# Performance work log

Measured on AMD Instinct MI355X. Metric: run time of the kernel, lower is better.

Reference implementation:

```python
import jax, jax.numpy as jnp
import numpy as np

DMODEL = 1024
DK = 64
DHEAD = 16
DEPTH = DK * DHEAD
N, LQ, L = 4, 4096, 4096
FAC1 = 1.0 / np.sqrt(DK)  # relu kernel scale folded into omega, as in reset()
EPS = 1e-6


def setup_inputs() -> dict:
    key = jax.random.key(0)
    ks = jax.random.split(key, 10)
    x = jax.random.normal(ks[0], (N, LQ, DMODEL), jnp.float32)
    y = jax.random.normal(ks[1], (N, L, DMODEL), jnp.float32)
    s_in = 1.0 / np.sqrt(DMODEL)
    s_depth = 1.0 / np.sqrt(DEPTH)
    # Linear weights stored as (in, out) so application is x @ W + b
    WQ = jax.random.normal(ks[2], (DMODEL, DEPTH), jnp.float32) * s_in
    WK = jax.random.normal(ks[3], (DMODEL, DEPTH), jnp.float32) * s_in
    WV = jax.random.normal(ks[4], (DMODEL, DEPTH), jnp.float32) * s_in
    WO = jax.random.normal(ks[5], (DEPTH, DMODEL), jnp.float32) * s_depth
    bQ = jnp.zeros((DEPTH,), jnp.float32)
    bK = jnp.zeros((DEPTH,), jnp.float32)
    bV = jnp.zeros((DEPTH,), jnp.float32)
    bO = jnp.zeros((DMODEL,), jnp.float32)
    # orthogonal random-feature projection: QR of gaussian, scaled by sqrt(dk), then *fac1 (relu)
    g = np.random.default_rng(0).standard_normal((DK, DK)).astype(np.float32)
    qmat, _ = np.linalg.qr(g)
    omega = jnp.asarray(qmat * np.sqrt(DK) * FAC1, dtype=jnp.float32)
    return dict(x=x, y=y, WQ=WQ, bQ=bQ, WK=WK, bK=bK, WV=WV, bV=bV,
                WO=WO, bO=bO, omega=omega)


def reference(x, y, WQ, bQ, WK, bK, WV, bV, WO, bO, omega):
    n, lq, _ = x.shape
    l = y.shape[1]
    # project and split heads: (n, h, L, dk)
    q = (x @ WQ + bQ).reshape(n, lq, DHEAD, DK).transpose(0, 2, 1, 3)
    k = (y @ WK + bK).reshape(n, l, DHEAD, DK).transpose(0, 2, 1, 3)
    v = (y @ WV + bV).reshape(n, l, DHEAD, DK).transpose(0, 2, 1, 3)
    # relu random-feature map phi(x) = relu(x @ omega) + eps
    q = jax.nn.relu(q @ omega) + EPS
    k = jax.nn.relu(k @ omega) + EPS
    # linear attention: out = phi(q) @ (phi(k)^T @ v) / (phi(q) @ phi(k)^T @ 1)
    kv = jnp.einsum('nhld,nhle->nhde', k, v)          # (n, h, dk, dk)
    ksum = jnp.sum(k, axis=2)                          # (n, h, dk)
    d_inv = jnp.einsum('nhqd,nhd->nhq', q, ksum)[..., None]
    out = jnp.einsum('nhqd,nhde->nhqe', q, kv) / d_inv  # (n, h, Lq, dk)
    out = out.transpose(0, 2, 1, 3).reshape(n, lq, DEPTH)
    return out @ WO + bO
```

## Files before the change

### kernel.cpp

```cpp
#include <hip/hip_runtime.h>

#define EPSF 1e-6f

typedef _Float16 f16x8 __attribute__((ext_vector_type(8)));
typedef _Float16 f16x4 __attribute__((ext_vector_type(4)));
typedef float    f32x4 __attribute__((ext_vector_type(4)));

#define GLL16(gp, lp) __builtin_amdgcn_global_load_lds( \
    (const __attribute__((address_space(1))) void*)(gp), \
    (__attribute__((address_space(3))) void*)(lp), 16, 0, 0)

__global__ __launch_bounds__(256) void cvt2_f16(const float* __restrict__ inA,
                                                _Float16* __restrict__ outA,
                                                const float* __restrict__ inB,
                                                _Float16* __restrict__ outB, int n8each) {
    int idx = blockIdx.x * 256 + threadIdx.x;
    const float* in = inA; _Float16* out = outA;
    if (idx >= n8each) { idx -= n8each; in = inB; out = outB; }
    const float4* p = (const float4*)in + (size_t)idx * 2;
    float4 a = p[0], b = p[1];
    f16x8 o;
    o[0] = (_Float16)a.x; o[1] = (_Float16)a.y; o[2] = (_Float16)a.z; o[3] = (_Float16)a.w;
    o[4] = (_Float16)b.x; o[5] = (_Float16)b.y; o[6] = (_Float16)b.z; o[7] = (_Float16)b.w;
    *(f16x8*)(out + (size_t)idx * 8) = o;
}

__global__ __launch_bounds__(256) void prep_all(const float* __restrict__ omega,
                                                const float* __restrict__ bQ,
                                                const float* __restrict__ bK,
                                                const float* __restrict__ bV,
                                                _Float16* __restrict__ obdT,
                                                float* __restrict__ bQf,
                                                float* __restrict__ bkv,
                                                float* __restrict__ ksum) {
    int idx = blockIdx.x * 256 + threadIdx.x;
    int c = idx >> 10, k = idx & 1023;
    float v = ((c >> 6) == (k >> 6)) ? omega[(k & 63) * 64 + (c & 63)] : 0.f;
    obdT[idx] = (_Float16)v;
    if (idx < 4096) ksum[idx] = 0.f;
    if (idx < 1024) {
        int h = idx >> 6, e = idx & 63;
        float sq = 0.f, sk = 0.f;
        for (int d = 0; d < 64; d++) {
            float o = omega[d * 64 + e];
            sq += bQ[h * 64 + d] * o;
            sk += bK[h * 64 + d] * o;
        }
        bQf[idx] = sq;
        bkv[h * 128 + e] = sk;
        bkv[h * 128 + 64 + e] = bV[idx];
    }
}

__global__ __launch_bounds__(256) void transpose_cvt(const float* __restrict__ in,
                                                     _Float16* __restrict__ out, int vmode) {
    __shared__ float tile[64][65];
    const int t = threadIdx.x;
    const int k0 = blockIdx.x * 64, n0 = blockIdx.y * 64;
#pragma unroll
    for (int j = 0; j < 16; j++) {
        int idx = j * 256 + t; int r = idx >> 6, c = idx & 63;
        tile[r][c] = in[(size_t)(k0 + r) * 1024 + n0 + c];
    }
    __syncthreads();
#pragma unroll
    for (int j = 0; j < 16; j++) {
        int idx = j * 256 + t; int rn = idx >> 6, ck = idx & 63;
        int rowo = n0 + rn;
        if (vmode) rowo = ((rowo >> 6) << 7) + 64 + (rowo & 63);
        out[(size_t)rowo * 1024 + k0 + ck] = (_Float16)tile[ck][rn];
    }
}

__global__ __launch_bounds__(256) void gemm_fold(const _Float16* __restrict__ A,
                                                 const _Float16* __restrict__ Bt,
                                                 _Float16* __restrict__ out0,
                                                 _Float16* __restrict__ out1) {
    const int K = 1024;
    __shared__ __align__(16) _Float16 Asm[128 * 32];
    __shared__ __align__(16) _Float16 Bsm[128 * 32];
    const int t = threadIdx.x, lane = t & 63, w = t >> 6;
    const int bm = blockIdx.y * 128, bn = blockIdx.x * 128;
    const int wm = (w >> 1) * 64, wn = (w & 1) * 64;
    const int r15 = lane & 15, slog = lane >> 4;

    int aoff[4], boff[4];
#pragma unroll
    for (int m = 0; m < 4; m++) {
        int ra = wm + m * 16 + r15;
        aoff[m] = ra * 32 + (slog ^ ((ra >> 1) & 3)) * 8;
        int rb = wn + m * 16 + r15;
        boff[m] = rb * 32 + (slog ^ ((rb >> 1) & 3)) * 8;
    }
    f32x4 acc[4][4];
#pragma unroll
    for (int m = 0; m < 4; m++)
#pragma unroll
        for (int n = 0; n < 4; n++) acc[m][n] = (f32x4){0.f, 0.f, 0.f, 0.f};

    for (int kt = 0; kt < K; kt += 32) {
        __syncthreads();
#pragma unroll
        for (int i = 0; i < 2; i++) {
            int seg = i * 256 + w * 64 + lane;
            int r = seg >> 2, sp = seg & 3;
            int sg = sp ^ ((r >> 1) & 3);
            GLL16(A  + (size_t)(bm + r) * K + kt + sg * 8, Asm + (size_t)(i * 256 + w * 64) * 8);
            GLL16(Bt + (size_t)(bn + r) * K + kt + sg * 8, Bsm + (size_t)(i * 256 + w * 64) * 8);
        }
        __syncthreads();
        f16x8 av[4], bv[4];
#pragma unroll
        for (int m = 0; m < 4; m++) av[m] = *(const f16x8*)(Asm + aoff[m]);
#pragma unroll
        for (int n = 0; n < 4; n++) bv[n] = *(const f16x8*)(Bsm + boff[n]);
#pragma unroll
        for (int m = 0; m < 4; m++)
#pragma unroll
            for (int n = 0; n < 4; n++)
                acc[m][n] = __builtin_amdgcn_mfma_f32_16x16x32_f16(av[m], bv[n], acc[m][n], 0, 0, 0);
    }

#pragma unroll
    for (int m = 0; m < 4; m++) {
        int row0 = bm + wm + m * 16 + slog * 4;
        int l = row0 & 1023;
#pragma unroll
        for (int n = 0; n < 4; n++) {
            int colg = bn + wn + n * 16 + r15;
            f16x4 p;
#pragma unroll
            for (int j = 0; j < 4; j++) p[j] = (_Float16)acc[m][n][j];
            if (row0 < 1024) {
                *(f16x4*)(out0 + (size_t)colg * 1024 + l) = p;
            } else {
                int rr = ((colg >> 6) << 7) + (colg & 63);
                *(f16x4*)(out1 + (size_t)rr * 1024 + l) = p;
            }
        }
    }
}

template<int EPI>
__global__ __launch_bounds__(512, 2) void gemm256(const _Float16* __restrict__ A,
                                                  const _Float16* __restrict__ Bt,
                                                  const float* __restrict__ bias,
                                                  void* __restrict__ out0,
                                                  void* __restrict__ out1,
                                                  float* __restrict__ ksum,
                                                  int M, int N, int K, int nbn) {
    __shared__ __align__(16) char lds[131072];
    const int t = threadIdx.x, lane = t & 63, w = t >> 6;
    const int nwg = gridDim.x;
    const int f = (blockIdx.x & 7) * (nwg >> 3) + (blockIdx.x >> 3);
    const int bm = (f / nbn) * 256, bn = (f % nbn) * 256;
    const int wm = (w & 1) * 128, wn = (w >> 1) * 64;
    const int r15 = lane & 15, hi = lane >> 4;
    const int srow = lane >> 2, sp = lane & 3;
    const _Float16* BtU = (EPI == 2) ? Bt + ((size_t)(bm >> 12) << 20) : Bt;

    int aoff[8], boff[4];
#pragma unroll
    for (int m = 0; m < 8; m++) {
        int r = wm + m * 16 + r15;
        aoff[m] = r * 64 + (((hi + (r >> 1)) & 3) << 4);
    }
#pragma unroll
    for (int n = 0; n < 4; n++) {
        int r = wn + n * 16 + r15;
        boff[n] = r * 64 + (((hi + (r >> 1)) & 3) << 4);
    }

    f32x4 acc[8][4];
#pragma unroll
    for (int m = 0; m < 8; m++)
#pragma unroll
        for (int n = 0; n < 4; n++) acc[m][n] = (f32x4){0.f, 0.f, 0.f, 0.f};

    auto stage = [&](int s) {
        char* base = lds + (s & 3) * 32768;
        int kt = s * 32;
#pragma unroll
        for (int p = 0; p < 2; p++) {
            int row = w * 32 + p * 16 + srow;
            int sg = (sp - ((row >> 1) & 3)) & 3;
            GLL16(A   + (size_t)(bm + row) * K + kt + sg * 8, base + w * 2048 + p * 1024);
            GLL16(BtU + (size_t)(bn + row) * K + kt + sg * 8, base + 16384 + w * 2048 + p * 1024);
        }
    };

    const int NS = K >> 5;
    stage(0); stage(1); stage(2);
    for (int s = 0; s < NS; ++s) {
        if (s + 2 < NS)      asm volatile("s_waitcnt vmcnt(8)" ::: "memory");
        else if (s + 1 < NS) asm volatile("s_waitcnt vmcnt(4)" ::: "memory");
        else                 asm volatile("s_waitcnt vmcnt(0)" ::: "memory");
        asm volatile("s_barrier" ::: "memory");
        if (s + 3 < NS) stage(s + 3);
        const char* La = lds + (s & 3) * 32768;
        const char* Lb = La + 16384;
        f16x8 bv[4];
#pragma unroll
        for (int n = 0; n < 4; n++) bv[n] = *(const f16x8*)(Lb + boff[n]);
        f16x8 av[8];
#pragma unroll
        for (int m = 0; m < 8; m++) av[m] = *(const f16x8*)(La + aoff[m]);
        __builtin_amdgcn_s_setprio(1);
#pragma unroll
        for (int m = 0; m < 8; m++)
#pragma unroll
            for (int n = 0; n < 4; n++)
                acc[m][n] = __builtin_amdgcn_mfma_f32_16x16x32_f16(av[m], bv[n], acc[m][n], 0, 0, 0);
        __builtin_amdgcn_s_setprio(0);
    }

    if (EPI == 5) {
        const int q = w >> 1;
        const bool isK = !(q & 1);
        const int nb = bm >> 12;
        const int g0 = bn >> 7;
        __syncthreads();
        char* LT = lds + q * 32768;
        float cs[4] = {0.f, 0.f, 0.f, 0.f};
#pragma unroll
        for (int m = 0; m < 8; m++)
#pragma unroll
            for (int n = 0; n < 4; n++) {
                int dd = n * 16 + r15;
                float bs = bias[bn + wn + dd];
                f16x4 pk;
#pragma unroll
                for (int j = 0; j < 4; j++) {
                    float xv = acc[m][n][j] + bs;
                    if (isK) { xv = fmaxf(xv, 0.f) + EPSF; cs[n] += xv; }
                    pk[j] = (_Float16)xv;
                }
                int l2 = (wm + m * 16 + hi * 4) * 2;
                *(f16x4*)(LT + dd * 512 + (l2 ^ ((dd & 7) << 4))) = pk;
            }
        if (isK) {
#pragma unroll
            for (int n = 0; n < 4; n++) {
                cs[n] += __shfl_xor(cs[n], 16, 64);
                cs[n] += __shfl_xor(cs[n], 32, 64);
            }
            if (hi == 0) {
#pragma unroll
                for (int n = 0; n < 4; n++)
                    atomicAdd(ksum + (size_t)(nb * 16 + g0 + (q >> 1)) * 64 + n * 16 + r15, cs[n]);
            }
        }
        __syncthreads();
        f32x4 kva[4];
#pragma unroll
        for (int i = 0; i < 4; i++) kva[i] = (f32x4){0.f, 0.f, 0.f, 0.f};
#pragma unroll
        for (int i = 0; i < 4; i++) {
            int tt = w * 4 + i;
            int hl = tt >> 4, dg = (tt >> 2) & 3, eg = tt & 3;
            const char* KT = lds + (hl * 2) * 32768;
            const char* VT = lds + (hl * 2 + 1) * 32768;
            int d = dg * 16 + r15, e = eg * 16 + r15;
#pragma unroll
            for (int ks = 0; ks < 8; ks++) {
                int l2 = (ks * 32 + hi * 8) * 2;
                f16x8 ka = *(const f16x8*)(KT + d * 512 + (l2 ^ ((d & 7) << 4)));
                f16x8 vb = *(const f16x8*)(VT + e * 512 + (l2 ^ ((e & 7) << 4)));
                kva[i] = __builtin_amdgcn_mfma_f32_16x16x32_f16(ka, vb, kva[i], 0, 0, 0);
            }
        }
        const int chunk = (bm >> 8) & 15;
        float* kvp = (float*)out0;
#pragma unroll
        for (int i = 0; i < 4; i++) {
            int tt = w * 4 + i;
            int hl = tt >> 4, dg = (tt >> 2) & 3, eg = tt & 3;
            float* dst = kvp + ((size_t)(nb * 16 + g0 + hl) * 16 + chunk) * 4096;
#pragma unroll
            for (int j = 0; j < 4; j++)
                dst[(dg * 16 + hi * 4 + j) * 64 + eg * 16 + r15] = kva[i][j];
        }
    } else if (EPI == 4) {
        const int headg = (bm >> 12) * 16 + ((bn + wn) >> 6);
        const float* ks = (const float*)out1;
        float ksn[4];
#pragma unroll
        for (int n = 0; n < 4; n++) ksn[n] = ks[(size_t)headg * 64 + n * 16 + r15];
        _Float16* C = (_Float16*)out0;
#pragma unroll
        for (int m = 0; m < 8; m++) {
            int row0 = bm + wm + m * 16 + hi * 4;
            float qv[4][4], dp[4] = {0.f, 0.f, 0.f, 0.f};
#pragma unroll
            for (int n = 0; n < 4; n++) {
                int colg = bn + wn + n * 16 + r15;
                float bs = bias[colg];
#pragma unroll
                for (int j = 0; j < 4; j++) {
                    float xv = fmaxf(acc[m][n][j] + bs, 0.f) + EPSF;
                    qv[n][j] = xv;
                    dp[j] += xv * ksn[n];
                }
            }
#pragma unroll
            for (int j = 0; j < 4; j++) {
                dp[j] += __shfl_xor(dp[j], 1, 64);
                dp[j] += __shfl_xor(dp[j], 2, 64);
                dp[j] += __shfl_xor(dp[j], 4, 64);
                dp[j] += __shfl_xor(dp[j], 8, 64);
                dp[j] = 4096.0f * __builtin_amdgcn_rcpf(dp[j]);
            }
#pragma unroll
            for (int n = 0; n < 4; n++) {
                int colg = bn + wn + n * 16 + r15;
#pragma unroll
                for (int j = 0; j < 4; j++)
                    C[(size_t)(row0 + j) * N + colg] = (_Float16)(qv[n][j] * dp[j]);
            }
        }
    } else {
#pragma unroll
        for (int m = 0; m < 8; m++) {
            int row0 = bm + wm + m * 16 + hi * 4;
#pragma unroll
            for (int n = 0; n < 4; n++) {
                int colg = bn + wn + n * 16 + r15;
                float bs = bias ? bias[colg] : 0.f;
#pragma unroll
                for (int j = 0; j < 4; j++)
                    ((float*)out0)[(size_t)(row0 + j) * N + colg] = acc[m][n][j] + bs;
            }
        }
    }
}

__global__ __launch_bounds__(256) void kvred16(const float* __restrict__ kvpart,
                                               float* __restrict__ kvT) {
    int gh = blockIdx.x, t = threadIdx.x;
    const float* kp = kvpart + (size_t)gh * 16 * 4096;
#pragma unroll
    for (int i = 0; i < 16; i++) {
        int idx = i * 256 + t;
        float s = 0.f;
#pragma unroll
        for (int c = 0; c < 16; c++) s += kp[c * 4096 + idx];
        kvT[(size_t)gh * 4096 + idx] = s;
    }
}

__global__ __launch_bounds__(256) void w2t_kernel(const _Float16* __restrict__ Wot,
                                                  const float* __restrict__ kvT,
                                                  _Float16* __restrict__ W2t) {
    const int t = threadIdx.x;
    const int jb = blockIdx.x;
    const int gh = blockIdx.y;
    const int b = gh >> 4, hl = gh & 15;
    __shared__ float kvL[64][65];
    const float* kp = kvT + (size_t)gh * 4096;
#pragma unroll
    for (int i = 0; i < 16; i++) {
        int idx = i * 256 + t;
        kvL[idx & 63][idx >> 6] = kp[idx];
    }
    __syncthreads();
    const int j = jb * 128 + (t >> 1);
    const int d0 = (t & 1) * 32;
    const _Float16* wr = Wot + (size_t)j * 1024 + hl * 64;
    float wv[64];
#pragma unroll
    for (int i = 0; i < 8; i++) {
        f16x8 v = *(const f16x8*)(wr + i * 8);
#pragma unroll
        for (int k = 0; k < 8; k++) wv[i * 8 + k] = (float)v[k];
    }
    _Float16* outp = W2t + ((size_t)b << 20) + (size_t)j * 1024 + hl * 64 + d0;
#pragma unroll
    for (int d = 0; d < 32; d++) {
        float s = 0.f;
#pragma unroll
        for (int e = 0; e < 64; e++) s += wv[e] * kvL[e][d0 + d];
        outp[d] = (_Float16)(s * (1.0f / 4096.0f));
    }
}

extern "C" void kernel_launch(void* const* d_in, const int* in_sizes, int n_in,
                              void* d_out, int out_size, void* d_ws, size_t ws_size,
                              hipStream_t stream) {
    (void)in_sizes; (void)n_in; (void)out_size; (void)ws_size;
    const float* x     = (const float*)d_in[0];
    const float* y     = (const float*)d_in[1];
    const float* WQ    = (const float*)d_in[2];
    const float* bQ    = (const float*)d_in[3];
    const float* WK    = (const float*)d_in[4];
    const float* bK    = (const float*)d_in[5];
    const float* WV    = (const float*)d_in[6];
    const float* bV    = (const float*)d_in[7];
    const float* WO    = (const float*)d_in[8];
    const float* bO    = (const float*)d_in[9];
    const float* omega = (const float*)d_in[10];

    char* ws = (char*)d_ws;
    size_t off = 0;
    auto alloc = [&](size_t bytes) { void* p = ws + off; off += (bytes + 255) & ~(size_t)255; return p; };
    const size_t BIG = (size_t)16384 * 1024 * 2;
    _Float16* xb    = (_Float16*)alloc(BIG);
    _Float16* yb    = (_Float16*)alloc(BIG);
    _Float16* WQKb  = (_Float16*)alloc((size_t)2048 * 1024 * 2);
    _Float16* obdT  = (_Float16*)alloc(1024 * 1024 * 2);
    _Float16* Wqt   = (_Float16*)alloc(1024 * 1024 * 2);
    _Float16* Wkvt  = (_Float16*)alloc((size_t)2048 * 1024 * 2);
    _Float16* Wot   = (_Float16*)alloc(1024 * 1024 * 2);
    _Float16* W2t   = (_Float16*)alloc((size_t)4 * 1024 * 1024 * 2);
    float*    bQf   = (float*)alloc(1024 * 4);
    float*    bkv   = (float*)alloc(2048 * 4);
    _Float16* U2    = (_Float16*)alloc(BIG);
    float*    kvpart= (float*)alloc((size_t)64 * 16 * 4096 * 4);
    float*    kvT   = (float*)alloc((size_t)64 * 4096 * 4);
    float*    ksum  = (float*)alloc((size_t)64 * 64 * 4);

    cvt2_f16<<<16384, 256, 0, stream>>>(x, xb, y, yb, 16384 * 1024 / 8);
    cvt2_f16<<<1024, 256, 0, stream>>>(WQ, WQKb, WK, WQKb + (size_t)1024 * 1024, 1024 * 1024 / 8);
    prep_all<<<4096, 256, 0, stream>>>(omega, bQ, bK, bV, obdT, bQf, bkv, ksum);
    transpose_cvt<<<dim3(16, 16), 256, 0, stream>>>(WV, Wkvt, 1);
    transpose_cvt<<<dim3(16, 16), 256, 0, stream>>>(WO, Wot, 0);
    gemm_fold<<<dim3(8, 16), 256, 0, stream>>>(WQKb, obdT, Wqt, Wkvt);
    gemm256<5><<<512, 512, 0, stream>>>(yb, Wkvt, bkv, kvpart, nullptr, ksum, 16384, 2048, 1024, 8);
    kvred16<<<64, 256, 0, stream>>>(kvpart, kvT);
    w2t_kernel<<<dim3(8, 64), 256, 0, stream>>>(Wot, kvT, W2t);
    gemm256<4><<<256, 512, 0, stream>>>(xb, Wqt, bQf, U2, ksum, nullptr, 16384, 1024, 1024, 4);
    gemm256<2><<<256, 512, 0, stream>>>(U2, W2t, bO, d_out, nullptr, nullptr, 16384, 1024, 1024, 4);
}
```

Measured before the change: 261.3 us.

## Shrink GEMM tile to 128x256 with double-buffered LDS for higher occupancy

Halves the M tile of the shared GEMM kernel from 256 to 128 rows, cuts LDS from 128KB to 48KB with a 2-stage instead of 4-stage pipeline, and raises launch bounds to allow more resident workgroups. Grid sizes double, and the fused KV epilogue is restructured to process two heads sequentially in reduced LDS, producing 32 partial chunks per head reduced by a new kvred32 kernel. The aim is better latency hiding via occupancy and more workgroups, at the cost of less data reuse per tile, a shallower prefetch pipeline with a full vmcnt(0) wait each step, and twice the partial-KV traffic.

Result: slower. 289.6 us (+10.8%).

```diff
diff --git a/kernel.cpp b/kernel.cpp
--- a/kernel.cpp
+++ b/kernel.cpp
@@ -142,26 +142,25 @@
 }
 
 template<int EPI>
-__global__ __launch_bounds__(512, 2) void gemm256(const _Float16* __restrict__ A,
+__global__ __launch_bounds__(512, 4) void gemm256(const _Float16* __restrict__ A,
                                                   const _Float16* __restrict__ Bt,
                                                   const float* __restrict__ bias,
                                                   void* __restrict__ out0,
                                                   void* __restrict__ out1,
                                                   float* __restrict__ ksum,
                                                   int M, int N, int K, int nbn) {
-    __shared__ __align__(16) char lds[131072];
+    __shared__ __align__(16) char lds[49152];
     const int t = threadIdx.x, lane = t & 63, w = t >> 6;
     const int nwg = gridDim.x;
     const int f = (blockIdx.x & 7) * (nwg >> 3) + (blockIdx.x >> 3);
-    const int bm = (f / nbn) * 256, bn = (f % nbn) * 256;
-    const int wm = (w & 1) * 128, wn = (w >> 1) * 64;
+    const int bm = (f / nbn) * 128, bn = (f % nbn) * 256;
+    const int wm = (w & 1) * 64, wn = (w >> 1) * 64;
     const int r15 = lane & 15, hi = lane >> 4;
-    const int srow = lane >> 2, sp = lane & 3;
     const _Float16* BtU = (EPI == 2) ? Bt + ((size_t)(bm >> 12) << 20) : Bt;
 
-    int aoff[8], boff[4];
-#pragma unroll
-    for (int m = 0; m < 8; m++) {
+    int aoff[4], boff[4];
+#pragma unroll
+    for (int m = 0; m < 4; m++) {
         int r = wm + m * 16 + r15;
         aoff[m] = r * 64 + (((hi + (r >> 1)) & 3) << 4);
     }
@@ -171,43 +170,45 @@
         boff[n] = r * 64 + (((hi + (r >> 1)) & 3) << 4);
     }
 
-    f32x4 acc[8][4];
-#pragma unroll
-    for (int m = 0; m < 8; m++)
+    f32x4 acc[4][4];
+#pragma unroll
+    for (int m = 0; m < 4; m++)
 #pragma unroll
         for (int n = 0; n < 4; n++) acc[m][n] = (f32x4){0.f, 0.f, 0.f, 0.f};
 
     auto stage = [&](int s) {
-        char* base = lds + (s & 3) * 32768;
+        char* base = lds + (s & 1) * 24576;
         int kt = s * 32;
+        {
+            int row = t >> 2;
+            int sg = ((t & 3) - ((row >> 1) & 3)) & 3;
+            GLL16(A + (size_t)(bm + row) * K + kt + sg * 8, base + (size_t)t * 16);
+        }
 #pragma unroll
         for (int p = 0; p < 2; p++) {
-            int row = w * 32 + p * 16 + srow;
-            int sg = (sp - ((row >> 1) & 3)) & 3;
-            GLL16(A   + (size_t)(bm + row) * K + kt + sg * 8, base + w * 2048 + p * 1024);
-            GLL16(BtU + (size_t)(bn + row) * K + kt + sg * 8, base + 16384 + w * 2048 + p * 1024);
+            int seg = p * 512 + t;
+            int row = seg >> 2;
+            int sg = ((seg & 3) - ((row >> 1) & 3)) & 3;
+            GLL16(BtU + (size_t)(bn + row) * K + kt + sg * 8, base + 8192 + (size_t)seg * 16);
         }
     };
 
     const int NS = K >> 5;
-    stage(0); stage(1); stage(2);
+    stage(0);
     for (int s = 0; s < NS; ++s) {
-        if (s + 2 < NS)      asm volatile("s_waitcnt vmcnt(8)" ::: "memory");
-        else if (s + 1 < NS) asm volatile("s_waitcnt vmcnt(4)" ::: "memory");
-        else                 asm volatile("s_waitcnt vmcnt(0)" ::: "memory");
+        asm volatile("s_waitcnt vmcnt(0)" ::: "memory");
         asm volatile("s_barrier" ::: "memory");
-        if (s + 3 < NS) stage(s + 3);
-        const char* La = lds + (s & 3) * 32768;
-        const char* Lb = La + 16384;
-        f16x8 bv[4];
+        if (s + 1 < NS) stage(s + 1);
+        const char* La = lds + (s & 1) * 24576;
+        const char* Lb = La + 8192;
+        f16x8 bv[4], av[4];
 #pragma unroll
         for (int n = 0; n < 4; n++) bv[n] = *(const f16x8*)(Lb + boff[n]);
-        f16x8 av[8];
-#pragma unroll
-        for (int m = 0; m < 8; m++) av[m] = *(const f16x8*)(La + aoff[m]);
+#pragma unroll
+        for (int m = 0; m < 4; m++) av[m] = *(const f16x8*)(La + aoff[m]);
         __builtin_amdgcn_s_setprio(1);
 #pragma unroll
-        for (int m = 0; m < 8; m++)
+        for (int m = 0; m < 4; m++)
 #pragma unroll
             for (int n = 0; n < 4; n++)
                 acc[m][n] = __builtin_amdgcn_mfma_f32_16x16x32_f16(av[m], bv[n], acc[m][n], 0, 0, 0);
@@ -215,70 +216,74 @@
     }
 
     if (EPI == 5) {
-        const int q = w >> 1;
-        const bool isK = !(q & 1);
         const int nb = bm >> 12;
         const int g0 = bn >> 7;
-        __syncthreads();
-        char* LT = lds + q * 32768;
-        float cs[4] = {0.f, 0.f, 0.f, 0.f};
-#pragma unroll
-        for (int m = 0; m < 8; m++)
-#pragma unroll
-            for (int n = 0; n < 4; n++) {
-                int dd = n * 16 + r15;
-                float bs = bias[bn + wn + dd];
-                f16x4 pk;
-#pragma unroll
-                for (int j = 0; j < 4; j++) {
-                    float xv = acc[m][n][j] + bs;
-                    if (isK) { xv = fmaxf(xv, 0.f) + EPSF; cs[n] += xv; }
-                    pk[j] = (_Float16)xv;
+        const int chunk = (bm >> 7) & 31;
+        const int cg = w >> 1;
+        const bool isK = (cg & 1) == 0;
+        asm volatile("s_waitcnt vmcnt(0)" ::: "memory");
+        for (int hp = 0; hp < 2; hp++) {
+            if (hp) { asm volatile("s_barrier" ::: "memory"); }
+            if ((w >> 2) == hp) {
+                char* LT = lds + (cg & 1) * 16384;
+                float cs[4] = {0.f, 0.f, 0.f, 0.f};
+#pragma unroll
+                for (int m = 0; m < 4; m++)
+#pragma unroll
+                    for (int n = 0; n < 4; n++) {
+                        int dd = n * 16 + r15;
+                        float bs = bias[bn + wn + dd];
+                        f16x4 pk;
+#pragma unroll
+                        for (int j = 0; j < 4; j++) {
+                            float xv = acc[m][n][j] + bs;
+                            if (isK) { xv = fmaxf(xv, 0.f) + EPSF; cs[n] += xv; }
+                            pk[j] = (_Float16)xv;
+                        }
+                        int l2 = (wm + m * 16 + hi * 4) * 2;
+                        *(f16x4*)(LT + dd * 256 + (l2 ^ ((dd & 15) << 4))) = pk;
+                    }
+                if (isK) {
+#pragma unroll
+                    for (int n = 0; n < 4; n++) {
+                        cs[n] += __shfl_xor(cs[n], 16, 64);
+                        cs[n] += __shfl_xor(cs[n], 32, 64);
+                    }
+                    if (hi == 0) {
+#pragma unroll
+                        for (int n = 0; n < 4; n++)
+                            atomicAdd(ksum + (size_t)(nb * 16 + g0 + hp) * 64 + n * 16 + r15, cs[n]);
+                    }
                 }
-                int l2 = (wm + m * 16 + hi * 4) * 2;
-                *(f16x4*)(LT + dd * 512 + (l2 ^ ((dd & 7) << 4))) = pk;
-            }
-        if (isK) {
-#pragma unroll
-            for (int n = 0; n < 4; n++) {
-                cs[n] += __shfl_xor(cs[n], 16, 64);
-                cs[n] += __shfl_xor(cs[n], 32, 64);
-            }
-            if (hi == 0) {
-#pragma unroll
-                for (int n = 0; n < 4; n++)
-                    atomicAdd(ksum + (size_t)(nb * 16 + g0 + (q >> 1)) * 64 + n * 16 + r15, cs[n]);
-            }
-        }
-        __syncthreads();
-        f32x4 kva[4];
-#pragma unroll
-        for (int i = 0; i < 4; i++) kva[i] = (f32x4){0.f, 0.f, 0.f, 0.f};
-#pragma unroll
-        for (int i = 0; i < 4; i++) {
-            int tt = w * 4 + i;
-            int hl = tt >> 4, dg = (tt >> 2) & 3, eg = tt & 3;
-            const char* KT = lds + (hl * 2) * 32768;
-            const char* VT = lds + (hl * 2 + 1) * 32768;
-            int d = dg * 16 + r15, e = eg * 16 + r15;
-#pragma unroll
-            for (int ks = 0; ks < 8; ks++) {
-                int l2 = (ks * 32 + hi * 8) * 2;
-                f16x8 ka = *(const f16x8*)(KT + d * 512 + (l2 ^ ((d & 7) << 4)));
-                f16x8 vb = *(const f16x8*)(VT + e * 512 + (l2 ^ ((e & 7) << 4)));
-                kva[i] = __builtin_amdgcn_mfma_f32_16x16x32_f16(ka, vb, kva[i], 0, 0, 0);
-            }
-        }
-        const int chunk = (bm >> 8) & 15;
-        float* kvp = (float*)out0;
-#pragma unroll
-        for (int i = 0; i < 4; i++) {
-            int tt = w * 4 + i;
-            int hl = tt >> 4, dg = (tt >> 2) & 3, eg = tt & 3;
-            float* dst = kvp + ((size_t)(nb * 16 + g0 + hl) * 16 + chunk) * 4096;
-#pragma unroll
-            for (int j = 0; j < 4; j++)
-                dst[(dg * 16 + hi * 4 + j) * 64 + eg * 16 + r15] = kva[i][j];
+            }
+            asm volatile("s_barrier" ::: "memory");
+            const char* KT = lds;
+            const char* VT = lds + 16384;
+            f32x4 kva[2];
+            kva[0] = (f32x4){0.f, 0.f, 0.f, 0.f};
+            kva[1] = (f32x4){0.f, 0.f, 0.f, 0.f};
+#pragma unroll
+            for (int i = 0; i < 2; i++) {
+                int tt = w * 2 + i;
+                int dg = tt >> 2, eg = tt & 3;
+                int d = dg * 16 + r15, e = eg * 16 + r15;
+#pragma unroll
+                for (int ks = 0; ks < 4; ks++) {
+                    int l2 = ks * 64 + hi * 16;
+                    f16x8 ka = *(const f16x8*)(KT + d * 256 + (l2 ^ ((d & 15) << 4)));
+                    f16x8 vb = *(const f16x8*)(VT + e * 256 + (l2 ^ ((e & 15) << 4)));
+                    kva[i] = __builtin_amdgcn_mfma_f32_16x16x32_f16(ka, vb, kva[i], 0, 0, 0);
+                }
+            }
+            float* dst = (float*)out0 + ((size_t)(nb * 16 + g0 + hp) * 32 + chunk) * 4096;
+#pragma unroll
+            for (int i = 0; i < 2; i++) {
+                int tt = w * 2 + i;
+                int dg = tt >> 2, eg = tt & 3;
+#pragma unroll
+                for (int j = 0; j < 4; j++)
+                    dst[(dg * 16 + hi * 4 + j) * 64 + eg * 16 + r15] = kva[i][j];
+            }
         }
     } else if (EPI == 4) {
         const int headg = (bm >> 12) * 16 + ((bn + wn) >> 6);
@@ -288,7 +293,7 @@
         for (int n = 0; n < 4; n++) ksn[n] = ks[(size_t)headg * 64 + n * 16 + r15];
         _Float16* C = (_Float16*)out0;
 #pragma unroll
-        for (int m = 0; m < 8; m++) {
+        for (int m = 0; m < 4; m++) {
             int row0 = bm + wm + m * 16 + hi * 4;
             float qv[4][4], dp[4] = {0.f, 0.f, 0.f, 0.f};
 #pragma unroll
@@ -320,7 +325,7 @@
         }
     } else {
 #pragma unroll
-        for (int m = 0; m < 8; m++) {
+        for (int m = 0; m < 4; m++) {
             int row0 = bm + wm + m * 16 + hi * 4;
 #pragma unroll
             for (int n = 0; n < 4; n++) {
@@ -334,16 +339,16 @@
     }
 }
 
-__global__ __launch_bounds__(256) void kvred16(const float* __restrict__ kvpart,
+__global__ __launch_bounds__(256) void kvred32(const float* __restrict__ kvpart,
                                                float* __restrict__ kvT) {
     int gh = blockIdx.x, t = threadIdx.x;
-    const float* kp = kvpart + (size_t)gh * 16 * 4096;
+    const float* kp = kvpart + (size_t)gh * 32 * 4096;
 #pragma unroll
     for (int i = 0; i < 16; i++) {
         int idx = i * 256 + t;
         float s = 0.f;
 #pragma unroll
-        for (int c = 0; c < 16; c++) s += kp[c * 4096 + idx];
+        for (int c = 0; c < 32; c++) s += kp[c * 4096 + idx];
         kvT[(size_t)gh * 4096 + idx] = s;
     }
 }
@@ -414,7 +419,7 @@
     float*    bQf   = (float*)alloc(1024 * 4);
     float*    bkv   = (float*)alloc(2048 * 4);
     _Float16* U2    = (_Float16*)alloc(BIG);
-    float*    kvpart= (float*)alloc((size_t)64 * 16 * 4096 * 4);
+    float*    kvpart= (float*)alloc((size_t)64 * 32 * 4096 * 4);
     float*    kvT   = (float*)alloc((size_t)64 * 4096 * 4);
     float*    ksum  = (float*)alloc((size_t)64 * 64 * 4);
 
@@ -424,9 +429,9 @@
     transpose_cvt<<<dim3(16, 16), 256, 0, stream>>>(WV, Wkvt, 1);
     transpose_cvt<<<dim3(16, 16), 256, 0, stream>>>(WO, Wot, 0);
     gemm_fold<<<dim3(8, 16), 256, 0, stream>>>(WQKb, obdT, Wqt, Wkvt);
-    gemm256<5><<<512, 512, 0, stream>>>(yb, Wkvt, bkv, kvpart, nullptr, ksum, 16384, 2048, 1024, 8);
-    kvred16<<<64, 256, 0, stream>>>(kvpart, kvT);
+    gemm256<5><<<1024, 512, 0, stream>>>(yb, Wkvt, bkv, kvpart, nullptr, ksum, 16384, 2048, 1024, 8);
+    kvred32<<<64, 256, 0, stream>>>(kvpart, kvT);
     w2t_kernel<<<dim3(8, 64), 256, 0, stream>>>(Wot, kvT, W2t);
-    gemm256<4><<<256, 512, 0, stream>>>(xb, Wqt, bQf, U2, ksum, nullptr, 16384, 1024, 1024, 4);
-    gemm256<2><<<256, 512, 0, stream>>>(U2, W2t, bO, d_out, nullptr, nullptr, 16384, 1024, 1024, 4);
-}
+    gemm256<4><<<512, 512, 0, stream>>>(xb, Wqt, bQf, U2, ksum, nullptr, 16384, 1024, 1024, 4);
+    gemm256<2><<<512, 512, 0, stream>>>(U2, W2t, bO, d_out, nullptr, nullptr, 16384, 1024, 1024, 4);
+}
```

## Restructure GEMM main loop into 8-wave ping-pong phases with split A/B staging

Applied to the files above, without the earlier changes.

Replaces the 4-stage 32-wide K pipeline with 64-wide K tiles that are double-buffered and split into A/B and K-half sub-stages. Each tile is processed in four phases that interleave LDS reads, issue of the next global-to-LDS loads, barriers, and an MFMA cluster over half the M fragments. The goal is to overlap memory issue with MFMA work more finely and to spread LDS traffic across phases. In exchange there are more barriers per K step, and the hand-written vmcnt accounting must match the number of loads in flight.

After: 269.1 us. 1.03x slower.

```diff
diff --git a/kernel.cpp b/kernel.cpp
--- a/kernel.cpp
+++ b/kernel.cpp
@@ -156,7 +156,6 @@
     const int bm = (f / nbn) * 256, bn = (f % nbn) * 256;
     const int wm = (w & 1) * 128, wn = (w >> 1) * 64;
     const int r15 = lane & 15, hi = lane >> 4;
-    const int srow = lane >> 2, sp = lane & 3;
     const _Float16* BtU = (EPI == 2) ? Bt + ((size_t)(bm >> 12) << 20) : Bt;
 
     int aoff[8], boff[4];
@@ -177,41 +176,61 @@
 #pragma unroll
         for (int n = 0; n < 4; n++) acc[m][n] = (f32x4){0.f, 0.f, 0.f, 0.f};
 
-    auto stage = [&](int s) {
-        char* base = lds + (s & 3) * 32768;
-        int kt = s * 32;
+    auto stage = [&](int T, int kh, int isB) {
+        const _Float16* src = isB ? BtU : A;
+        const int brow = isB ? bn : bm;
+        char* base = lds + isB * 65536 + (T & 1) * 32768 + kh * 16384;
+        const int kt = T * 64 + kh * 32;
 #pragma unroll
         for (int p = 0; p < 2; p++) {
-            int row = w * 32 + p * 16 + srow;
-            int sg = (sp - ((row >> 1) & 3)) & 3;
-            GLL16(A   + (size_t)(bm + row) * K + kt + sg * 8, base + w * 2048 + p * 1024);
-            GLL16(BtU + (size_t)(bn + row) * K + kt + sg * 8, base + 16384 + w * 2048 + p * 1024);
+            int seg = p * 512 + t;
+            int row = seg >> 2;
+            int sg = ((seg & 3) - ((row >> 1) & 3)) & 3;
+            GLL16(src + (size_t)(brow + row) * K + kt + sg * 8, base + (size_t)seg * 16);
         }
     };
 
-    const int NS = K >> 5;
-    stage(0); stage(1); stage(2);
-    for (int s = 0; s < NS; ++s) {
-        if (s + 2 < NS)      asm volatile("s_waitcnt vmcnt(8)" ::: "memory");
-        else if (s + 1 < NS) asm volatile("s_waitcnt vmcnt(4)" ::: "memory");
-        else                 asm volatile("s_waitcnt vmcnt(0)" ::: "memory");
-        asm volatile("s_barrier" ::: "memory");
-        if (s + 3 < NS) stage(s + 3);
-        const char* La = lds + (s & 3) * 32768;
-        const char* Lb = La + 16384;
-        f16x8 bv[4];
-#pragma unroll
-        for (int n = 0; n < 4; n++) bv[n] = *(const f16x8*)(Lb + boff[n]);
-        f16x8 av[8];
-#pragma unroll
-        for (int m = 0; m < 8; m++) av[m] = *(const f16x8*)(La + aoff[m]);
-        __builtin_amdgcn_s_setprio(1);
-#pragma unroll
-        for (int m = 0; m < 8; m++)
-#pragma unroll
-            for (int n = 0; n < 4; n++)
-                acc[m][n] = __builtin_amdgcn_mfma_f32_16x16x32_f16(av[m], bv[n], acc[m][n], 0, 0, 0);
-        __builtin_amdgcn_s_setprio(0);
+    const int NT = K >> 6;
+    stage(0, 0, 0); stage(0, 0, 1); stage(0, 1, 0); stage(0, 1, 1);
+    stage(1, 0, 0); stage(1, 0, 1);
+    asm volatile("s_waitcnt vmcnt(4)" ::: "memory");
+    asm volatile("s_barrier" ::: "memory");
+
+    for (int T = 0; T < NT; ++T) {
+        const int b = T & 1;
+        const bool s1 = (T + 1 < NT), s2 = (T + 2 < NT);
+#pragma unroll
+        for (int ph = 0; ph < 4; ph++) {
+            const int kh = ph >> 1, mh = ph & 1;
+            const char* RA = lds + b * 32768 + kh * 16384;
+            const char* RB = RA + 65536;
+            f16x8 av[4], bv[4];
+#pragma unroll
+            for (int i = 0; i < 4; i++) av[i] = *(const f16x8*)(RA + aoff[mh * 4 + i]);
+#pragma unroll
+            for (int n = 0; n < 4; n++) bv[n] = *(const f16x8*)(RB + boff[n]);
+            if (ph == 0)      { if (s1) stage(T + 1, 1, 0); }
+            else if (ph == 1) { if (s1) stage(T + 1, 1, 1); }
+            else if (ph == 2) { if (s2) stage(T + 2, 0, 0); }
+            else {
+                if (s2) {
+                    stage(T + 2, 0, 1);
+                    asm volatile("s_waitcnt vmcnt(4)" ::: "memory");
+                } else {
+                    asm volatile("s_waitcnt vmcnt(0)" ::: "memory");
+                }
+            }
+            asm volatile("s_barrier" ::: "memory");
+            asm volatile("s_waitcnt lgkmcnt(0)" ::: "memory");
+            __builtin_amdgcn_s_setprio(1);
+#pragma unroll
+            for (int i = 0; i < 4; i++)
+#pragma unroll
+                for (int n = 0; n < 4; n++)
+                    acc[mh * 4 + i][n] = __builtin_amdgcn_mfma_f32_16x16x32_f16(av[i], bv[n], acc[mh * 4 + i][n], 0, 0, 0);
+            __builtin_amdgcn_s_setprio(0);
+            asm volatile("s_barrier" ::: "memory");
+        }
     }
 
     if (EPI == 5) {
```
